# Kernel tuning notes

Hardware: AMD Instinct MI355X
Metric: run time of the kernel (lower is better)

## Reference

```python
import jax, jax.numpy as jnp
import numpy as np
import math

DIM = 768          # hyena_config.dim * (order - 1)
EMB = 33           # positional embedding dim (odd)
BANDS = (EMB - 1) // 2
FO = 64            # filter_order (MLP width)
LMAX = 8192
SHIFT = 0.05
FAST_DECAY = 0.3
SLOW_DECAY = 1.5
TARGET = 0.01


def next_power_of_2(x):
    return 2 ** math.ceil(math.log2(x))


def setup_inputs() -> dict:
    key = jax.random.key(0)
    ks = jax.random.split(key, 10)
    s = 1.0 / math.sqrt(EMB)
    sf = 1.0 / math.sqrt(FO)
    return {
        "x": jax.random.normal(ks[0], (2, DIM, LMAX), dtype=jnp.float32),
        "W0": jax.random.uniform(ks[1], (EMB, FO), jnp.float32, -s, s),
        "b0": jax.random.uniform(ks[2], (FO,), jnp.float32, -s, s),
        "W1": jax.random.uniform(ks[3], (FO, FO), jnp.float32, -sf, sf),
        "b1": jax.random.uniform(ks[4], (FO,), jnp.float32, -sf, sf),
        "W2": jax.random.uniform(ks[5], (FO, FO), jnp.float32, -sf, sf),
        "b2": jax.random.uniform(ks[6], (FO,), jnp.float32, -sf, sf),
        "Wf": jax.random.uniform(ks[7], (FO, DIM), jnp.float32, -sf, sf),
        "freq": jnp.ones((1, FO), dtype=jnp.float32),  # HyenaSin freq (activation_freq=1.0)
        "bias": jax.random.normal(ks[8], (DIM,), dtype=jnp.float32),
        "L": LMAX,
    }


def _implicit_filter(L, W0, b0, W1, b1, W2, b2, Wf, freq):
    # PositionalEmbedding buffers (constants)
    t = jnp.linspace(0.0, 1.0, L)[None, :, None]                    # [1, L, 1]
    t_rescaled = jnp.linspace(0.0, L - 1, L)[None, :, None]
    w = 2.0 * jnp.pi * t_rescaled / L                               # [1, L, 1]
    f = jnp.linspace(1e-4, BANDS - 1, BANDS)[None, None]            # [1, 1, bands]
    zc = jnp.exp(-1j * f * w)                                       # [1, L, bands] complex
    z = jnp.concatenate([t, zc.real, zc.imag], axis=-1)             # [1, L, EMB]
    # implicit filter MLP with sin activation
    h = jnp.sin(freq * (z @ W0 + b0))
    h = jnp.sin(freq * (h @ W1 + b1))
    h = jnp.sin(freq * (h @ W2 + b2))
    h = h @ Wf                                                      # [1, L, DIM]
    # ExponentialModulation
    max_decay = math.log(TARGET) / FAST_DECAY
    min_decay = math.log(TARGET) / SLOW_DECAY
    deltas = jnp.linspace(min_decay, max_decay, DIM)[None, None]    # [1, 1, DIM]
    decay = jnp.exp(-t * jnp.abs(deltas))                           # [1, L, DIM]
    h = h * (decay + SHIFT)
    return h[0].T                                                   # [DIM, L]


def _fftconv(u, k, D):
    # u: [B, d, L], k: [d, L], D: [d]
    seqlen = u.shape[-1]
    fft_size = next_power_of_2(2 * seqlen)
    k_f = jnp.fft.rfft(k, n=fft_size) / fft_size                    # [d, F]
    u_f = jnp.fft.rfft(u, n=fft_size)                               # [B, d, F]
    y = jnp.fft.irfft(u_f * k_f, n=fft_size, norm="forward")[..., :seqlen]
    return (y + u * D[:, None]).astype(u.dtype)


def reference(x, W0, b0, W1, b1, W2, b2, Wf, freq, bias, L):
    k = _implicit_filter(L, W0, b0, W1, b1, W2, b2, Wf, freq)       # [DIM, L]
    return _fftconv(x, k, bias)
```

## Files before the change

kernel.cpp:

```cpp
#include <hip/hip_runtime.h>
#include <hip/hip_fp16.h>


#define DIMC  768
#define BANDS 16
#define FO    64
#define LSEQ  8192
#define NF    16384
#define PI_F  3.14159265358979323846f
#define RSQ2  0.70710678118654752f

typedef float v2f __attribute__((ext_vector_type(2)));

#define REP32(M) M(0) M(1) M(2) M(3) M(4) M(5) M(6) M(7) M(8) M(9) M(10) M(11) \
    M(12) M(13) M(14) M(15) M(16) M(17) M(18) M(19) M(20) M(21) M(22) M(23) \
    M(24) M(25) M(26) M(27) M(28) M(29) M(30) M(31)

__device__ __forceinline__ int swz(int i) { return i ^ ((i >> 4) & 15); }

__device__ __forceinline__ v2f mni(v2f v) { v2f t = v.yx; t.y = -t.y; return t; }
__device__ __forceinline__ v2f pli(v2f v) { v2f t = v.yx; t.x = -t.x; return t; }
__device__ __forceinline__ v2f cmulm(v2f x, float c, float s) {
    v2f t = x.yx; t.y = -t.y;
    return x * c + t * s;
}
__device__ __forceinline__ v2f cmulp(v2f x, float c, float s) {
    v2f t = x.yx; t.x = -t.x;
    return x * c + t * s;
}

#define TWCHAIN7(TH) \
    float c1=__cosf(TH), s1=__sinf(TH); \
    float c2=c1*c1-s1*s1, s2=2.f*c1*s1; \
    float c3=c1*c2-s1*s2, s3=s1*c2+c1*s2; \
    float c4=c2*c2-s2*s2, s4=2.f*c2*s2; \
    float c5=c2*c3-s2*s3, s5=s2*c3+c2*s3; \
    float c6=c3*c3-s3*s3, s6=2.f*c3*s3; \
    float c7=c3*c4-s3*s4, s7=s3*c4+c3*s4

template<int SH>
__device__ __forceinline__ void fwd8_stage(v2f* L, int t)
{
    __syncthreads();
    const int S = 1 << SH;
#pragma unroll 1
    for (int m = 0; m < 2; ++m) {
        int b = t + (m << 10);
        int q = b & (S - 1);
        int p = ((b >> SH) << (SH + 3)) + q;
        v2f u0 = L[swz(p)];
        v2f u1 = L[swz(p + S)];
        v2f u2 = L[swz(p + 2 * S)];
        v2f u3 = L[swz(p + 3 * S)];
        v2f u4 = L[swz(p + 4 * S)];
        v2f u5 = L[swz(p + 5 * S)];
        v2f u6 = L[swz(p + 6 * S)];
        v2f u7 = L[swz(p + 7 * S)];
        v2f a0 = u0 + u4, b0 = u0 - u4;
        v2f a1 = u1 + u5, b1 = u1 - u5;
        v2f a2 = u2 + u6, b2 = u2 - u6;
        v2f a3 = u3 + u7, b3 = u3 - u7;
        v2f e0 = a0 + a2, e1 = a0 - a2;
        v2f f0 = a1 + a3, f1 = a1 - a3;
        v2f y0 = e0 + f0, y4 = e0 - f0;
        v2f nf1 = mni(f1);
        v2f y2 = e1 + nf1, y6 = e1 - nf1;
        v2f v1 = cmulm(b1,  RSQ2, RSQ2);
        v2f v2 = mni(b2);
        v2f v3 = cmulm(b3, -RSQ2, RSQ2);
        v2f g0 = b0 + v2, g1 = b0 - v2;
        v2f h0 = v1 + v3, h1 = v1 - v3;
        v2f y1 = g0 + h0, y5 = g0 - h0;
        v2f nh1 = mni(h1);
        v2f y3 = g1 + nh1, y7 = g1 - nh1;
        float th = (float)q * (PI_F / (4.0f * (float)S));
        TWCHAIN7(th);
        L[swz(p)]         = y0;
        L[swz(p + S)]     = cmulm(y1, c1, s1);
        L[swz(p + 2 * S)] = cmulm(y2, c2, s2);
        L[swz(p + 3 * S)] = cmulm(y3, c3, s3);
        L[swz(p + 4 * S)] = cmulm(y4, c4, s4);
        L[swz(p + 5 * S)] = cmulm(y5, c5, s5);
        L[swz(p + 6 * S)] = cmulm(y6, c6, s6);
        L[swz(p + 7 * S)] = cmulm(y7, c7, s7);
    }
}

__device__ __forceinline__ void fwd8_first(v2f* L, int q,
                                           v2f u0, v2f u1, v2f u2, v2f u3)
{
    v2f e0 = u0 + u2, e1 = u0 - u2;
    v2f f0 = u1 + u3, f1 = u1 - u3;
    v2f y0 = e0 + f0, y4 = e0 - f0;
    v2f nf1 = mni(f1);
    v2f y2 = e1 + nf1, y6 = e1 - nf1;
    v2f v1 = cmulm(u1,  RSQ2, RSQ2);
    v2f v2 = mni(u2);
    v2f v3 = cmulm(u3, -RSQ2, RSQ2);
    v2f g0 = u0 + v2, g1 = u0 - v2;
    v2f h0 = v1 + v3, h1 = v1 - v3;
    v2f y1 = g0 + h0, y5 = g0 - h0;
    v2f nh1 = mni(h1);
    v2f y3 = g1 + nh1, y7 = g1 - nh1;
    float th = (float)q * (PI_F / 8192.0f);
    TWCHAIN7(th);
    L[swz(q)]         = y0;
    L[swz(q + 2048)]  = cmulm(y1, c1, s1);
    L[swz(q + 4096)]  = cmulm(y2, c2, s2);
    L[swz(q + 6144)]  = cmulm(y3, c3, s3);
    L[swz(q + 8192)]  = cmulm(y4, c4, s4);
    L[swz(q + 10240)] = cmulm(y5, c5, s5);
    L[swz(q + 12288)] = cmulm(y6, c6, s6);
    L[swz(q + 14336)] = cmulm(y7, c7, s7);
}

template<int SH>
__device__ __forceinline__ void inv8_stage(v2f* L, int t)
{
    __syncthreads();
    const int S = 1 << SH;
#pragma unroll 1
    for (int m = 0; m < 2; ++m) {
        int b = t + (m << 10);
        int q = b & (S - 1);
        int p = ((b >> SH) << (SH + 3)) + q;
        float th = (float)q * (PI_F / (4.0f * (float)S));
        TWCHAIN7(th);
        v2f y0 = L[swz(p)];
        v2f y1 = cmulp(L[swz(p + S)],     c1, s1);
        v2f y2 = cmulp(L[swz(p + 2*S)],   c2, s2);
        v2f y3 = cmulp(L[swz(p + 3*S)],   c3, s3);
        v2f y4 = cmulp(L[swz(p + 4*S)],   c4, s4);
        v2f y5 = cmulp(L[swz(p + 5*S)],   c5, s5);
        v2f y6 = cmulp(L[swz(p + 6*S)],   c6, s6);
        v2f y7 = cmulp(L[swz(p + 7*S)],   c7, s7);
        v2f E0 = y0 + y4, F0 = y0 - y4;
        v2f E1 = y2 + y6, F1 = pli(y2 - y6);
        v2f a0 = E0 + E1, a2 = E0 - E1;
        v2f a1 = F0 + F1, a3 = F0 - F1;
        v2f G0 = y1 + y5, H0 = y1 - y5;
        v2f G1 = y3 + y7, H1 = pli(y3 - y7);
        v2f w0 = G0 + G1, w2 = G0 - G1;
        v2f w1 = H0 + H1, w3 = H0 - H1;
        v2f b0 = w0;
        v2f b1 = cmulp(w1,  RSQ2, RSQ2);
        v2f b2 = pli(w2);
        v2f b3 = cmulp(w3, -RSQ2, RSQ2);
        L[swz(p)]         = a0 + b0;
        L[swz(p + S)]     = a1 + b1;
        L[swz(p + 2 * S)] = a2 + b2;
        L[swz(p + 3 * S)] = a3 + b3;
        L[swz(p + 4 * S)] = a0 - b0;
        L[swz(p + 5 * S)] = a1 - b1;
        L[swz(p + 6 * S)] = a2 - b2;
        L[swz(p + 7 * S)] = a3 - b3;
    }
}

__device__ __forceinline__ void bf4f0(v2f& a, v2f& b, v2f& c, v2f& d)
{
    v2f A = a + c, B = a - c, C = b + d, D = mni(b - d);
    a = A + C; b = B + D; c = A - C; d = B - D;
}
__device__ __forceinline__ void bf4i0(v2f& a, v2f& b, v2f& c, v2f& d)
{
    v2f e0 = a + c, e1 = a - c, f0 = b + d, f1 = pli(b - d);
    a = e0 + f0; b = e1 + f1; c = e0 - f0; d = e1 - f1;
}

__global__ void hidden_kernel(const float* __restrict__ W0, const float* __restrict__ b0,
                              const float* __restrict__ W1, const float* __restrict__ b1,
                              const float* __restrict__ W2, const float* __restrict__ b2,
                              const float* __restrict__ freq, float* __restrict__ hws)
{
    const int lane = threadIdx.x & 63;
    const int p = blockIdx.x * (blockDim.x >> 6) + (threadIdx.x >> 6);
    if (p >= LSEQ) return;
    const float tt = (float)p / (float)(LSEQ - 1);
    const float w  = 6.283185307179586f * (float)p / (float)LSEQ;

    float acc = b0[lane] + tt * W0[lane];
#pragma unroll
    for (int j = 0; j < BANDS; ++j) {
        float f = 1e-4f + (float)j * ((15.0f - 1e-4f) / 15.0f);
        float a = f * w;
        acc += __cosf(a)  * W0[(1 + j) * FO + lane];
        acc += -__sinf(a) * W0[(1 + BANDS + j) * FO + lane];
    }
    float h = __sinf(freq[lane] * acc);

    acc = b1[lane];
#pragma unroll
    for (int e = 0; e < FO; ++e) acc += __shfl(h, e) * W1[e * FO + lane];
    float h1 = __sinf(freq[lane] * acc);

    acc = b2[lane];
#pragma unroll
    for (int e = 0; e < FO; ++e) acc += __shfl(h1, e) * W2[e * FO + lane];
    float h2 = __sinf(freq[lane] * acc);

    hws[lane * LSEQ + p] = h2;
}

#define DCHUNK 96
__global__ __launch_bounds__(256)
void filter_kernel(const float* __restrict__ hws, const float* __restrict__ Wf,
                   float* __restrict__ kws)
{
    __shared__ float hsh[FO][257];
    const int tid = threadIdx.x;
    const int p  = blockIdx.x * 256 + tid;
    const int d0 = blockIdx.y * DCHUNK;
#pragma unroll 1
    for (int j = 0; j < FO; ++j) hsh[j][tid] = hws[j * LSEQ + p];
    __syncthreads();
    const float tt = (float)p / (float)(LSEQ - 1);
    const float min_decay = -3.0701134573253937f;
    const float max_decay = -15.350567286626971f;
#pragma unroll 1
    for (int c = 0; c < DCHUNK / 32; ++c) {
        const int dc = d0 + c * 32;
#define DEFA(I) float a##I = 0.f;
        REP32(DEFA)
#undef DEFA
#pragma unroll 4
        for (int j = 0; j < FO; ++j) {
            float hj = hsh[j][tid];
            const float* Wj = Wf + j * DIMC + dc;
#define FMA_(I) a##I = fmaf(hj, Wj[I], a##I);
            REP32(FMA_)
#undef FMA_
        }
#define ST_(I) { int d = dc + I; \
    float delta = min_decay + (max_decay - min_decay) * ((float)d / (float)(DIMC - 1)); \
    float dec = __expf(-tt * fabsf(delta)); \
    kws[(size_t)d * LSEQ + p] = a##I * (dec + 0.05f); }
        REP32(ST_)
#undef ST_
    }
}

template<int MODE>
__global__ __launch_bounds__(1024)
void kfft_kernel(const float* __restrict__ kf, const float* __restrict__ bias,
                 __half2* __restrict__ KF, float* __restrict__ outbase)
{
    __shared__ v2f L[NF];
    const int g = blockIdx.x, t = threadIdx.x;
    const int da = 2 * g, db = 2 * g + 1;
    const float* ka = kf + (size_t)da * LSEQ;
    const float* kb = kf + (size_t)db * LSEQ;
#pragma unroll 1
    for (int m = 0; m < 2; ++m) {
        int q = t + (m << 10);
        float vr = ka[q], vi = kb[q];
        if (q == 0) { vr += bias[da]; vi += bias[db]; }
        fwd8_first(L, q, (v2f){vr, vi},
                   (v2f){ka[q + 2048], kb[q + 2048]},
                   (v2f){ka[q + 4096], kb[q + 4096]},
                   (v2f){ka[q + 6144], kb[q + 6144]});
    }
    fwd8_stage<8>(L, t);
    fwd8_stage<5>(L, t);
    fwd8_stage<2>(L, t);
    __syncthreads();
#pragma unroll 1
    for (int ch = 0; ch < 2; ++ch) {
        int n0 = (t << 4) + (ch << 3);
        v2f z0 = L[swz(n0)],     z1 = L[swz(n0 + 1)];
        v2f z2 = L[swz(n0 + 2)], z3 = L[swz(n0 + 3)];
        v2f z4 = L[swz(n0 + 4)], z5 = L[swz(n0 + 5)];
        v2f z6 = L[swz(n0 + 6)], z7 = L[swz(n0 + 7)];
        bf4f0(z0, z1, z2, z3); bf4f0(z4, z5, z6, z7);
        L[swz(n0)]     = z0; L[swz(n0 + 1)] = z1;
        L[swz(n0 + 2)] = z2; L[swz(n0 + 3)] = z3;
        L[swz(n0 + 4)] = z4; L[swz(n0 + 5)] = z5;
        L[swz(n0 + 6)] = z6; L[swz(n0 + 7)] = z7;
    }
    __syncthreads();
    const float hn = 0.5f / 16384.f;
#pragma unroll 1
    for (int i = 0; i < 16; ++i) {
        int s = (i << 10) + t;
        int D0 = s >> 11, D1 = (s >> 8) & 7, D2 = (s >> 5) & 7, D3 = (s >> 2) & 7, E = s & 3;
        int n  = D0 + (D1 << 3) + (D2 << 6) + (D3 << 9) + (E << 12);
        int np = (16384 - n) & 16383;
        int sp = ((np & 7) << 11) | (((np >> 3) & 7) << 8) | (((np >> 6) & 7) << 5)
               | (((np >> 9) & 7) << 2) | ((np >> 12) & 3);
        v2f Zs = L[swz(s)];
        v2f Zp = L[swz(sp)];
        float kar = (Zs.x + Zp.x) * hn, kai = (Zs.y - Zp.y) * hn;
        float kbr = (Zs.y + Zp.y) * hn, kbi = (Zp.x - Zs.x) * hn;
        if (MODE == 0) {
            KF[(size_t)da * NF + s] = __floats2half2_rn(kar, kai);
            KF[(size_t)db * NF + s] = __floats2half2_rn(kbr, kbi);
        } else {
            __half2* Ha = (s < 8192)
                ? (__half2*)(outbase + (size_t)da * LSEQ) + s
                : (__half2*)(outbase + (size_t)(DIMC + da) * LSEQ) + (s - 8192);
            __half2* Hb = (s < 8192)
                ? (__half2*)(outbase + (size_t)db * LSEQ) + s
                : (__half2*)(outbase + (size_t)(DIMC + db) * LSEQ) + (s - 8192);
            *Ha = __floats2half2_rn(kar, kai);
            *Hb = __floats2half2_rn(kbr, kbi);
        }
    }
}

template<int MODE>
__global__ __launch_bounds__(1024)
void conv_kernel(const float* __restrict__ x, const __half2* __restrict__ KF,
                 float* __restrict__ out)
{
    __shared__ v2f L[NF];
    const int d = blockIdx.x, t = threadIdx.x;
    const float* x0 = x + (size_t)d * LSEQ;
    const float* x1 = x + (size_t)(DIMC + d) * LSEQ;
    float* o0 = out + (size_t)d * LSEQ;
    float* o1 = out + (size_t)(DIMC + d) * LSEQ;
#pragma unroll 1
    for (int m = 0; m < 2; ++m) {
        int q = t + (m << 10);
        fwd8_first(L, q, (v2f){x0[q], x1[q]},
                   (v2f){x0[q + 2048], x1[q + 2048]},
                   (v2f){x0[q + 4096], x1[q + 4096]},
                   (v2f){x0[q + 6144], x1[q + 6144]});
    }
    fwd8_stage<8>(L, t);
    fwd8_stage<5>(L, t);
    fwd8_stage<2>(L, t);
    __syncthreads();
#pragma unroll 1
    for (int ch = 0; ch < 2; ++ch) {
        int n0 = (t << 4) + (ch << 3);
        v2f z0 = L[swz(n0)],     z1 = L[swz(n0 + 1)];
        v2f z2 = L[swz(n0 + 2)], z3 = L[swz(n0 + 3)];
        v2f z4 = L[swz(n0 + 4)], z5 = L[swz(n0 + 5)];
        v2f z6 = L[swz(n0 + 6)], z7 = L[swz(n0 + 7)];
        bf4f0(z0, z1, z2, z3); bf4f0(z4, z5, z6, z7);
        const __half2* H;
        if (MODE == 0) H = KF + (size_t)d * NF + n0;
        else H = (n0 < 8192)
            ? (const __half2*)(out + (size_t)d * LSEQ) + n0
            : (const __half2*)(out + (size_t)(DIMC + d) * LSEQ) + (n0 - 8192);
#define KMH(Z, J) { float2 kk = __half22float2(H[J]); v2f k = {kk.x, kk.y}; \
    Z = k * Z.x + pli(k) * Z.y; }
        KMH(z0,0) KMH(z1,1) KMH(z2,2) KMH(z3,3) KMH(z4,4) KMH(z5,5) KMH(z6,6) KMH(z7,7)
#undef KMH
        bf4i0(z0, z1, z2, z3); bf4i0(z4, z5, z6, z7);
        L[swz(n0)]     = z0; L[swz(n0 + 1)] = z1;
        L[swz(n0 + 2)] = z2; L[swz(n0 + 3)] = z3;
        L[swz(n0 + 4)] = z4; L[swz(n0 + 5)] = z5;
        L[swz(n0 + 6)] = z6; L[swz(n0 + 7)] = z7;
    }
    inv8_stage<2>(L, t);
    inv8_stage<5>(L, t);
    inv8_stage<8>(L, t);
    __syncthreads();
#pragma unroll 1
    for (int m = 0; m < 2; ++m) {
        int q = t + (m << 10);
        float th = (float)q * (PI_F / 8192.0f);
        TWCHAIN7(th);
        v2f y0 = L[swz(q)];
        v2f y1 = cmulp(L[swz(q + 2048)],  c1, s1);
        v2f y2 = cmulp(L[swz(q + 4096)],  c2, s2);
        v2f y3 = cmulp(L[swz(q + 6144)],  c3, s3);
        v2f y4 = cmulp(L[swz(q + 8192)],  c4, s4);
        v2f y5 = cmulp(L[swz(q + 10240)], c5, s5);
        v2f y6 = cmulp(L[swz(q + 12288)], c6, s6);
        v2f y7 = cmulp(L[swz(q + 14336)], c7, s7);
        v2f E0 = y0 + y4, F0 = y0 - y4;
        v2f E1 = y2 + y6, F1 = pli(y2 - y6);
        v2f a0 = E0 + E1, a2 = E0 - E1;
        v2f a1 = F0 + F1, a3 = F0 - F1;
        v2f G0 = y1 + y5, H0 = y1 - y5;
        v2f G1 = y3 + y7, H1 = pli(y3 - y7);
        v2f w0 = G0 + G1, w2 = G0 - G1;
        v2f w1 = H0 + H1, w3 = H0 - H1;
        v2f b0 = w0;
        v2f b1 = cmulp(w1,  RSQ2, RSQ2);
        v2f b2 = pli(w2);
        v2f b3 = cmulp(w3, -RSQ2, RSQ2);
        v2f r0 = a0 + b0, r1 = a1 + b1, r2 = a2 + b2, r3 = a3 + b3;
        o0[q]        = r0.x;  o1[q]        = r0.y;
        o0[q + 2048] = r1.x;  o1[q + 2048] = r1.y;
        o0[q + 4096] = r2.x;  o1[q + 4096] = r2.y;
        o0[q + 6144] = r3.x;  o1[q + 6144] = r3.y;
    }
}

extern "C" void kernel_launch(void* const* d_in, const int* in_sizes, int n_in,
                              void* d_out, int out_size, void* d_ws, size_t ws_size,
                              hipStream_t stream)
{
    (void)in_sizes; (void)n_in; (void)out_size;
    const float* x    = (const float*)d_in[0];
    const float* W0   = (const float*)d_in[1];
    const float* b0   = (const float*)d_in[2];
    const float* W1   = (const float*)d_in[3];
    const float* b1   = (const float*)d_in[4];
    const float* W2   = (const float*)d_in[5];
    const float* b2   = (const float*)d_in[6];
    const float* Wf   = (const float*)d_in[7];
    const float* freq = (const float*)d_in[8];
    const float* bias = (const float*)d_in[9];
    float* out = (float*)d_out;

    float* hws = out;
    float* kws = out + (size_t)DIMC * LSEQ;

    hipLaunchKernelGGL(hidden_kernel, dim3(LSEQ / 4), dim3(256), 0, stream,
                       W0, b0, W1, b1, W2, b2, freq, hws);
    hipLaunchKernelGGL(filter_kernel, dim3(LSEQ / 256, DIMC / DCHUNK), dim3(256), 0, stream,
                       hws, Wf, kws);

    const size_t kbytes = (size_t)DIMC * NF * sizeof(__half2);
    if (ws_size >= kbytes) {
        __half2* KF = (__half2*)d_ws;
        hipLaunchKernelGGL(kfft_kernel<0>, dim3(DIMC / 2), dim3(1024), 0, stream,
                           kws, bias, KF, nullptr);
        hipLaunchKernelGGL(conv_kernel<0>, dim3(DIMC), dim3(1024), 0, stream,
                           x, KF, out);
    } else {
        hipLaunchKernelGGL(kfft_kernel<1>, dim3(DIMC / 2), dim3(1024), 0, stream,
                           kws, bias, nullptr, out);
        hipLaunchKernelGGL(conv_kernel<1>, dim3(DIMC), dim3(1024), 0, stream,
                           x, nullptr, out);
    }
}
```

Before: 158.0 us.

## Replace 16384-point FFT convolution with block-split 8192-point FFTs

```diff
diff --git a/kernel.cpp b/kernel.cpp
--- a/kernel.cpp
+++ b/kernel.cpp
@@ -27,6 +27,11 @@
 __device__ __forceinline__ v2f cmulp(v2f x, float c, float s) {
     v2f t = x.yx; t.x = -t.x;
     return x * c + t * s;
+}
+__device__ __forceinline__ v2f kmul(__half2 kh, v2f z) {
+    float2 kk = __half22float2(kh);
+    v2f k = {kk.x, kk.y};
+    return k * z.x + pli(k) * z.y;
 }
 
 #define TWCHAIN7(TH) \
@@ -38,13 +43,13 @@
     float c6=c3*c3-s3*s3, s6=2.f*c3*s3; \
     float c7=c3*c4-s3*s4, s7=s3*c4+c3*s4
 
-template<int SH>
-__device__ __forceinline__ void fwd8_stage(v2f* L, int t)
+template<int SH, int MIT>
+__device__ __forceinline__ void fwd8s(v2f* L, int t)
 {
     __syncthreads();
     const int S = 1 << SH;
 #pragma unroll 1
-    for (int m = 0; m < 2; ++m) {
+    for (int m = 0; m < MIT; ++m) {
         int b = t + (m << 10);
         int q = b & (S - 1);
         int p = ((b >> SH) << (SH + 3)) + q;
@@ -86,6 +91,7 @@
     }
 }
 
+template<int NS>
 __device__ __forceinline__ void fwd8_first(v2f* L, int q,
                                            v2f u0, v2f u1, v2f u2, v2f u3)
 {
@@ -102,25 +108,25 @@
     v2f y1 = g0 + h0, y5 = g0 - h0;
     v2f nh1 = mni(h1);
     v2f y3 = g1 + nh1, y7 = g1 - nh1;
-    float th = (float)q * (PI_F / 8192.0f);
+    float th = (float)q * (PI_F / (4.0f * (float)NS));
     TWCHAIN7(th);
-    L[swz(q)]         = y0;
-    L[swz(q + 2048)]  = cmulm(y1, c1, s1);
-    L[swz(q + 4096)]  = cmulm(y2, c2, s2);
-    L[swz(q + 6144)]  = cmulm(y3, c3, s3);
-    L[swz(q + 8192)]  = cmulm(y4, c4, s4);
-    L[swz(q + 10240)] = cmulm(y5, c5, s5);
-    L[swz(q + 12288)] = cmulm(y6, c6, s6);
-    L[swz(q + 14336)] = cmulm(y7, c7, s7);
-}
-
-template<int SH>
-__device__ __forceinline__ void inv8_stage(v2f* L, int t)
+    L[swz(q)]          = y0;
+    L[swz(q + NS)]     = cmulm(y1, c1, s1);
+    L[swz(q + 2 * NS)] = cmulm(y2, c2, s2);
+    L[swz(q + 3 * NS)] = cmulm(y3, c3, s3);
+    L[swz(q + 4 * NS)] = cmulm(y4, c4, s4);
+    L[swz(q + 5 * NS)] = cmulm(y5, c5, s5);
+    L[swz(q + 6 * NS)] = cmulm(y6, c6, s6);
+    L[swz(q + 7 * NS)] = cmulm(y7, c7, s7);
+}
+
+template<int SH, int MIT>
+__device__ __forceinline__ void inv8s(v2f* L, int t)
 {
     __syncthreads();
     const int S = 1 << SH;
 #pragma unroll 1
-    for (int m = 0; m < 2; ++m) {
+    for (int m = 0; m < MIT; ++m) {
         int b = t + (m << 10);
         int q = b & (S - 1);
         int p = ((b >> SH) << (SH + 3)) + q;
@@ -240,10 +246,202 @@
     }
 }
 
-template<int MODE>
 __global__ __launch_bounds__(1024)
-void kfft_kernel(const float* __restrict__ kf, const float* __restrict__ bias,
-                 __half2* __restrict__ KF, float* __restrict__ outbase)
+void kfft8_kernel(const float* __restrict__ kf, const float* __restrict__ bias,
+                  __half2* __restrict__ KF)
+{
+    __shared__ v2f L[8192];
+    const int d = blockIdx.x, t = threadIdx.x;
+    const float* kr = kf + (size_t)d * LSEQ;
+    {
+        float r0 = kr[t]; if (t == 0) r0 += bias[d];
+        fwd8_first<1024>(L, t,
+            (v2f){r0,            kr[4096 + t]},
+            (v2f){kr[t + 1024],  kr[5120 + t]},
+            (v2f){kr[t + 2048],  kr[6144 + t]},
+            (v2f){kr[t + 3072],  kr[7168 + t]});
+    }
+    fwd8s<7, 1>(L, t);
+    fwd8s<4, 1>(L, t);
+    fwd8s<1, 1>(L, t);
+    __syncthreads();
+    {
+        int n0 = t << 3;
+        v2f z0 = L[swz(n0)],     z1 = L[swz(n0 + 1)];
+        v2f z2 = L[swz(n0 + 2)], z3 = L[swz(n0 + 3)];
+        v2f z4 = L[swz(n0 + 4)], z5 = L[swz(n0 + 5)];
+        v2f z6 = L[swz(n0 + 6)], z7 = L[swz(n0 + 7)];
+        L[swz(n0)]     = z0 + z1; L[swz(n0 + 1)] = z0 - z1;
+        L[swz(n0 + 2)] = z2 + z3; L[swz(n0 + 3)] = z2 - z3;
+        L[swz(n0 + 4)] = z4 + z5; L[swz(n0 + 5)] = z4 - z5;
+        L[swz(n0 + 6)] = z6 + z7; L[swz(n0 + 7)] = z6 - z7;
+    }
+    __syncthreads();
+    const float hn = 0.5f / 8192.f;
+    __half2* K0 = KF + (size_t)d * 16384;
+    __half2* K1 = K0 + 8192;
+#pragma unroll 1
+    for (int i = 0; i < 8; ++i) {
+        int s = (i << 10) + t;
+        int f0 = s >> 10, f1 = (s >> 7) & 7, f2 = (s >> 4) & 7, f3 = (s >> 1) & 7, g = s & 1;
+        int n  = f0 + (f1 << 3) + (f2 << 6) + (f3 << 9) + (g << 12);
+        int np = (8192 - n) & 8191;
+        int sp = ((np & 7) << 10) | (((np >> 3) & 7) << 7) | (((np >> 6) & 7) << 4)
+               | (((np >> 9) & 7) << 1) | (np >> 12);
+        v2f Zs = L[swz(s)];
+        v2f Zp = L[swz(sp)];
+        K0[s] = __floats2half2_rn((Zs.x + Zp.x) * hn, (Zs.y - Zp.y) * hn);
+        K1[s] = __floats2half2_rn((Zs.y + Zp.y) * hn, (Zp.x - Zs.x) * hn);
+    }
+}
+
+__global__ __launch_bounds__(1024)
+void conv8_kernel(const float* __restrict__ x, const __half2* __restrict__ KF,
+                  float* __restrict__ out)
+{
+    __shared__ v2f L[8192];
+    const int d = blockIdx.x, t = threadIdx.x;
+    const float* x0 = x + (size_t)d * LSEQ;
+    const float* x1 = x + (size_t)(DIMC + d) * LSEQ;
+    float* o0 = out + (size_t)d * LSEQ;
+    float* o1 = out + (size_t)(DIMC + d) * LSEQ;
+    const __half2* K0 = KF + (size_t)d * 16384;
+    const __half2* K1 = K0 + 8192;
+    v2f C0, C1, C2, C3, C4, C5, C6, C7;
+
+    fwd8_first<1024>(L, t,
+        (v2f){x0[t],        x1[t]},
+        (v2f){x0[t + 1024], x1[t + 1024]},
+        (v2f){x0[t + 2048], x1[t + 2048]},
+        (v2f){x0[t + 3072], x1[t + 3072]});
+    fwd8s<7, 1>(L, t);
+    fwd8s<4, 1>(L, t);
+    fwd8s<1, 1>(L, t);
+    __syncthreads();
+    {
+        int n0 = t << 3;
+        v2f z0 = L[swz(n0)],     z1 = L[swz(n0 + 1)];
+        v2f z2 = L[swz(n0 + 2)], z3 = L[swz(n0 + 3)];
+        v2f z4 = L[swz(n0 + 4)], z5 = L[swz(n0 + 5)];
+        v2f z6 = L[swz(n0 + 6)], z7 = L[swz(n0 + 7)];
+        v2f w0 = z0 + z1, w1 = z0 - z1, w2 = z2 + z3, w3 = z2 - z3;
+        v2f w4 = z4 + z5, w5 = z4 - z5, w6 = z6 + z7, w7 = z6 - z7;
+        v2f A0 = kmul(K0[n0],     w0), A1 = kmul(K0[n0 + 1], w1);
+        v2f A2 = kmul(K0[n0 + 2], w2), A3 = kmul(K0[n0 + 3], w3);
+        v2f A4 = kmul(K0[n0 + 4], w4), A5 = kmul(K0[n0 + 5], w5);
+        v2f A6 = kmul(K0[n0 + 6], w6), A7 = kmul(K0[n0 + 7], w7);
+        C0 = kmul(K1[n0],     w0); C1 = kmul(K1[n0 + 1], w1);
+        C2 = kmul(K1[n0 + 2], w2); C3 = kmul(K1[n0 + 3], w3);
+        C4 = kmul(K1[n0 + 4], w4); C5 = kmul(K1[n0 + 5], w5);
+        C6 = kmul(K1[n0 + 6], w6); C7 = kmul(K1[n0 + 7], w7);
+        L[swz(n0)]     = A0 + A1; L[swz(n0 + 1)] = A0 - A1;
+        L[swz(n0 + 2)] = A2 + A3; L[swz(n0 + 3)] = A2 - A3;
+        L[swz(n0 + 4)] = A4 + A5; L[swz(n0 + 5)] = A4 - A5;
+        L[swz(n0 + 6)] = A6 + A7; L[swz(n0 + 7)] = A6 - A7;
+    }
+    inv8s<1, 1>(L, t);
+    inv8s<4, 1>(L, t);
+    inv8s<7, 1>(L, t);
+    __syncthreads();
+    {
+        float th = (float)t * (PI_F / 4096.0f);
+        TWCHAIN7(th);
+        v2f y0 = L[swz(t)];
+        v2f y1 = cmulp(L[swz(t + 1024)], c1, s1);
+        v2f y2 = cmulp(L[swz(t + 2048)], c2, s2);
+        v2f y3 = cmulp(L[swz(t + 3072)], c3, s3);
+        v2f y4 = cmulp(L[swz(t + 4096)], c4, s4);
+        v2f y5 = cmulp(L[swz(t + 5120)], c5, s5);
+        v2f y6 = cmulp(L[swz(t + 6144)], c6, s6);
+        v2f y7 = cmulp(L[swz(t + 7168)], c7, s7);
+        v2f E0 = y0 + y4, F0 = y0 - y4;
+        v2f E1 = y2 + y6, F1 = pli(y2 - y6);
+        v2f a0 = E0 + E1, a2 = E0 - E1;
+        v2f a1 = F0 + F1, a3 = F0 - F1;
+        v2f G0 = y1 + y5, H0 = y1 - y5;
+        v2f G1 = y3 + y7, H1 = pli(y3 - y7);
+        v2f w0 = G0 + G1, w2 = G0 - G1;
+        v2f w1 = H0 + H1, w3 = H0 - H1;
+        v2f b0 = w0;
+        v2f b1 = cmulp(w1,  RSQ2, RSQ2);
+        v2f b2 = pli(w2);
+        v2f b3 = cmulp(w3, -RSQ2, RSQ2);
+        v2f r0 = a0 + b0, r1 = a1 + b1, r2 = a2 + b2, r3 = a3 + b3;
+        v2f r4 = a0 - b0, r5 = a1 - b1, r6 = a2 - b2, r7 = a3 - b3;
+        o0[t]        = r0.x; o1[t]        = r0.y;
+        o0[t + 1024] = r1.x; o1[t + 1024] = r1.y;
+        o0[t + 2048] = r2.x; o1[t + 2048] = r2.y;
+        o0[t + 3072] = r3.x; o1[t + 3072] = r3.y;
+        o0[t + 4096] = r4.x; o1[t + 4096] = r4.y;
+        o0[t + 5120] = r5.x; o1[t + 5120] = r5.y;
+        o0[t + 6144] = r6.x; o1[t + 6144] = r6.y;
+        o0[t + 7168] = r7.x; o1[t + 7168] = r7.y;
+    }
+    __syncthreads();
+    fwd8_first<1024>(L, t,
+        (v2f){x0[4096 + t],        x1[4096 + t]},
+        (v2f){x0[5120 + t],        x1[5120 + t]},
+        (v2f){x0[6144 + t],        x1[6144 + t]},
+        (v2f){x0[7168 + t],        x1[7168 + t]});
+    fwd8s<7, 1>(L, t);
+    fwd8s<4, 1>(L, t);
+    fwd8s<1, 1>(L, t);
+    __syncthreads();
+    {
+        int n0 = t << 3;
+        v2f z0 = L[swz(n0)],     z1 = L[swz(n0 + 1)];
+        v2f z2 = L[swz(n0 + 2)], z3 = L[swz(n0 + 3)];
+        v2f z4 = L[swz(n0 + 4)], z5 = L[swz(n0 + 5)];
+        v2f z6 = L[swz(n0 + 6)], z7 = L[swz(n0 + 7)];
+        v2f w0 = z0 + z1, w1 = z0 - z1, w2 = z2 + z3, w3 = z2 - z3;
+        v2f w4 = z4 + z5, w5 = z4 - z5, w6 = z6 + z7, w7 = z6 - z7;
+        v2f B0 = kmul(K0[n0],     w0) + C0, B1 = kmul(K0[n0 + 1], w1) + C1;
+        v2f B2 = kmul(K0[n0 + 2], w2) + C2, B3 = kmul(K0[n0 + 3], w3) + C3;
+        v2f B4 = kmul(K0[n0 + 4], w4) + C4, B5 = kmul(K0[n0 + 5], w5) + C5;
+        v2f B6 = kmul(K0[n0 + 6], w6) + C6, B7 = kmul(K0[n0 + 7], w7) + C7;
+        L[swz(n0)]     = B0 + B1; L[swz(n0 + 1)] = B0 - B1;
+        L[swz(n0 + 2)] = B2 + B3; L[swz(n0 + 3)] = B2 - B3;
+        L[swz(n0 + 4)] = B4 + B5; L[swz(n0 + 5)] = B4 - B5;
+        L[swz(n0 + 6)] = B6 + B7; L[swz(n0 + 7)] = B6 - B7;
+    }
+    inv8s<1, 1>(L, t);
+    inv8s<4, 1>(L, t);
+    inv8s<7, 1>(L, t);
+    __syncthreads();
+    {
+        float th = (float)t * (PI_F / 4096.0f);
+        TWCHAIN7(th);
+        v2f y0 = L[swz(t)];
+        v2f y1 = cmulp(L[swz(t + 1024)], c1, s1);
+        v2f y2 = cmulp(L[swz(t + 2048)], c2, s2);
+        v2f y3 = cmulp(L[swz(t + 3072)], c3, s3);
+        v2f y4 = cmulp(L[swz(t + 4096)], c4, s4);
+        v2f y5 = cmulp(L[swz(t + 5120)], c5, s5);
+        v2f y6 = cmulp(L[swz(t + 6144)], c6, s6);
+        v2f y7 = cmulp(L[swz(t + 7168)], c7, s7);
+        v2f E0 = y0 + y4;
+        v2f E1 = y2 + y6, F0 = y0 - y4, F1 = pli(y2 - y6);
+        v2f a0 = E0 + E1, a2 = E0 - E1;
+        v2f a1 = F0 + F1, a3 = F0 - F1;
+        v2f G0 = y1 + y5, H0 = y1 - y5;
+        v2f G1 = y3 + y7, H1 = pli(y3 - y7);
+        v2f w0 = G0 + G1, w2 = G0 - G1;
+        v2f w1 = H0 + H1, w3 = H0 - H1;
+        v2f b0 = w0;
+        v2f b1 = cmulp(w1,  RSQ2, RSQ2);
+        v2f b2 = pli(w2);
+        v2f b3 = cmulp(w3, -RSQ2, RSQ2);
+        v2f r0 = a0 + b0, r1 = a1 + b1, r2 = a2 + b2, r3 = a3 + b3;
+        o0[4096 + t] += r0.x;  o1[4096 + t] += r0.y;
+        o0[5120 + t] += r1.x;  o1[5120 + t] += r1.y;
+        o0[6144 + t] += r2.x;  o1[6144 + t] += r2.y;
+        o0[7168 + t] += r3.x;  o1[7168 + t] += r3.y;
+    }
+}
+
+__global__ __launch_bounds__(1024)
+void kfft_kernel1(const float* __restrict__ kf, const float* __restrict__ bias,
+                  float* __restrict__ outbase)
 {
     __shared__ v2f L[NF];
     const int g = blockIdx.x, t = threadIdx.x;
@@ -255,14 +453,14 @@
         int q = t + (m << 10);
         float vr = ka[q], vi = kb[q];
         if (q == 0) { vr += bias[da]; vi += bias[db]; }
-        fwd8_first(L, q, (v2f){vr, vi},
+        fwd8_first<2048>(L, q, (v2f){vr, vi},
                    (v2f){ka[q + 2048], kb[q + 2048]},
                    (v2f){ka[q + 4096], kb[q + 4096]},
                    (v2f){ka[q + 6144], kb[q + 6144]});
     }
-    fwd8_stage<8>(L, t);
-    fwd8_stage<5>(L, t);
-    fwd8_stage<2>(L, t);
+    fwd8s<8, 2>(L, t);
+    fwd8s<5, 2>(L, t);
+    fwd8s<2, 2>(L, t);
     __syncthreads();
 #pragma unroll 1
     for (int ch = 0; ch < 2; ++ch) {
@@ -291,26 +489,19 @@
         v2f Zp = L[swz(sp)];
         float kar = (Zs.x + Zp.x) * hn, kai = (Zs.y - Zp.y) * hn;
         float kbr = (Zs.y + Zp.y) * hn, kbi = (Zp.x - Zs.x) * hn;
-        if (MODE == 0) {
-            KF[(size_t)da * NF + s] = __floats2half2_rn(kar, kai);
-            KF[(size_t)db * NF + s] = __floats2half2_rn(kbr, kbi);
-        } else {
-            __half2* Ha = (s < 8192)
-                ? (__half2*)(outbase + (size_t)da * LSEQ) + s
-                : (__half2*)(outbase + (size_t)(DIMC + da) * LSEQ) + (s - 8192);
-            __half2* Hb = (s < 8192)
-                ? (__half2*)(outbase + (size_t)db * LSEQ) + s
-                : (__half2*)(outbase + (size_t)(DIMC + db) * LSEQ) + (s - 8192);
-            *Ha = __floats2half2_rn(kar, kai);
-            *Hb = __floats2half2_rn(kbr, kbi);
-        }
-    }
-}
-
-template<int MODE>
+        __half2* Ha = (s < 8192)
+            ? (__half2*)(outbase + (size_t)da * LSEQ) + s
+            : (__half2*)(outbase + (size_t)(DIMC + da) * LSEQ) + (s - 8192);
+        __half2* Hb = (s < 8192)
+            ? (__half2*)(outbase + (size_t)db * LSEQ) + s
+            : (__half2*)(outbase + (size_t)(DIMC + db) * LSEQ) + (s - 8192);
+        *Ha = __floats2half2_rn(kar, kai);
+        *Hb = __floats2half2_rn(kbr, kbi);
+    }
+}
+
 __global__ __launch_bounds__(1024)
-void conv_kernel(const float* __restrict__ x, const __half2* __restrict__ KF,
-                 float* __restrict__ out)
+void conv_kernel1(const float* __restrict__ x, float* __restrict__ out)
 {
     __shared__ v2f L[NF];
     const int d = blockIdx.x, t = threadIdx.x;
@@ -321,14 +512,14 @@
 #pragma unroll 1
     for (int m = 0; m < 2; ++m) {
         int q = t + (m << 10);
-        fwd8_first(L, q, (v2f){x0[q], x1[q]},
+        fwd8_first<2048>(L, q, (v2f){x0[q], x1[q]},
                    (v2f){x0[q + 2048], x1[q + 2048]},
                    (v2f){x0[q + 4096], x1[q + 4096]},
                    (v2f){x0[q + 6144], x1[q + 6144]});
     }
-    fwd8_stage<8>(L, t);
-    fwd8_stage<5>(L, t);
-    fwd8_stage<2>(L, t);
+    fwd8s<8, 2>(L, t);
+    fwd8s<5, 2>(L, t);
+    fwd8s<2, 2>(L, t);
     __syncthreads();
 #pragma unroll 1
     for (int ch = 0; ch < 2; ++ch) {
@@ -338,24 +529,22 @@
         v2f z4 = L[swz(n0 + 4)], z5 = L[swz(n0 + 5)];
         v2f z6 = L[swz(n0 + 6)], z7 = L[swz(n0 + 7)];
         bf4f0(z0, z1, z2, z3); bf4f0(z4, z5, z6, z7);
-        const __half2* H;
-        if (MODE == 0) H = KF + (size_t)d * NF + n0;
-        else H = (n0 < 8192)
+        const __half2* H = (n0 < 8192)
             ? (const __half2*)(out + (size_t)d * LSEQ) + n0
             : (const __half2*)(out + (size_t)(DIMC + d) * LSEQ) + (n0 - 8192);
-#define KMH(Z, J) { float2 kk = __half22float2(H[J]); v2f k = {kk.x, kk.y}; \
-    Z = k * Z.x + pli(k) * Z.y; }
-        KMH(z0,0) KMH(z1,1) KMH(z2,2) KMH(z3,3) KMH(z4,4) KMH(z5,5) KMH(z6,6) KMH(z7,7)
-#undef KMH
+        z0 = kmul(H[0], z0); z1 = kmul(H[1], z1);
+        z2 = kmul(H[2], z2); z3 = kmul(H[3], z3);
+        z4 = kmul(H[4], z4); z5 = kmul(H[5], z5);
+        z6 = kmul(H[6], z6); z7 = kmul(H[7], z7);
         bf4i0(z0, z1, z2, z3); bf4i0(z4, z5, z6, z7);
         L[swz(n0)]     = z0; L[swz(n0 + 1)] = z1;
         L[swz(n0 + 2)] = z2; L[swz(n0 + 3)] = z3;
         L[swz(n0 + 4)] = z4; L[swz(n0 + 5)] = z5;
         L[swz(n0 + 6)] = z6; L[swz(n0 + 7)] = z7;
     }
-    inv8_stage<2>(L, t);
-    inv8_stage<5>(L, t);
-    inv8_stage<8>(L, t);
+    inv8s<2, 2>(L, t);
+    inv8s<5, 2>(L, t);
+    inv8s<8, 2>(L, t);
     __syncthreads();
 #pragma unroll 1
     for (int m = 0; m < 2; ++m) {
@@ -415,17 +604,17 @@
     hipLaunchKernelGGL(filter_kernel, dim3(LSEQ / 256, DIMC / DCHUNK), dim3(256), 0, stream,
                        hws, Wf, kws);
 
-    const size_t kbytes = (size_t)DIMC * NF * sizeof(__half2);
+    const size_t kbytes = (size_t)DIMC * 2 * 8192 * sizeof(__half2);
     if (ws_size >= kbytes) {
         __half2* KF = (__half2*)d_ws;
-        hipLaunchKernelGGL(kfft_kernel<0>, dim3(DIMC / 2), dim3(1024), 0, stream,
-                           kws, bias, KF, nullptr);
-        hipLaunchKernelGGL(conv_kernel<0>, dim3(DIMC), dim3(1024), 0, stream,
+        hipLaunchKernelGGL(kfft8_kernel, dim3(DIMC), dim3(1024), 0, stream,
+                           kws, bias, KF);
+        hipLaunchKernelGGL(conv8_kernel, dim3(DIMC), dim3(1024), 0, stream,
                            x, KF, out);
     } else {
-        hipLaunchKernelGGL(kfft_kernel<1>, dim3(DIMC / 2), dim3(1024), 0, stream,
-                           kws, bias, nullptr, out);
-        hipLaunchKernelGGL(conv_kernel<1>, dim3(DIMC), dim3(1024), 0, stream,
-                           x, nullptr, out);
-    }
-}
+        hipLaunchKernelGGL(kfft_kernel1, dim3(DIMC / 2), dim3(1024), 0, stream,
+                           kws, bias, out);
+        hipLaunchKernelGGL(conv_kernel1, dim3(DIMC), dim3(1024), 0, stream,
+                           x, out);
+    }
+}
```

Result: slower. 320.7 us (+103.1%).
